# Kernel optimization log

Hardware: AMD Instinct MI355X
Metric: run time of the kernel (lower is better)

## Reference

```python
import jax, jax.numpy as jnp
import numpy as np

H, D = 16, 64  # heads, head dim; E = H*D


def setup_inputs() -> dict:
    key = jax.random.key(0)
    ks = jax.random.split(key, 8)
    B, T, E = 4, 1024, 1024
    s = (2.0 / E) ** 0.5
    return {
        "x": jax.random.normal(ks[0], (B, T, E), jnp.float32),
        "wq": jax.random.normal(ks[1], (H * D, E), jnp.float32) * s,
        "wk": jax.random.normal(ks[2], (H * D, E), jnp.float32) * s,
        "wv": jax.random.normal(ks[3], (H * D, E), jnp.float32) * s,
        "wvr": jax.random.normal(ks[4], (H * D, E), jnp.float32) * s,
        "wr": jax.random.normal(ks[5], (H, E, T), jnp.float32) * s,
        "wj": jax.random.normal(ks[6], (E, E), jnp.float32) * s,
        "gate": jnp.zeros((H, 3), jnp.float32),
        "wo": jax.random.normal(ks[7], (E, H * D), jnp.float32) * s,
    }


def reference(x, wq, wk, wv, wvr, wr, wj, gate, wo):
    B, T, E = x.shape
    scale = 1.0 / D ** 0.5

    def proj(w):  # torch Linear: y = x @ w.T, then split heads -> (B,H,T,D)
        return jnp.einsum('bte,fe->btf', x, w).reshape(B, T, H, D).transpose(0, 2, 1, 3)

    mask = jnp.triu(jnp.ones((T, T), bool), 1)  # True above diagonal (masked)

    # --- branch 1: standard causal QKV attention ---
    q, k, v = proj(wq), proj(wk), proj(wv)
    s1 = jnp.einsum('bhid,bhjd->bhij', q, k) * scale
    a1 = jax.nn.softmax(jnp.where(mask, -jnp.inf, s1), axis=-1)
    out1 = jnp.einsum('bhij,bhjd->bhid', a1, v)

    # --- branch 2: RRPRAM (parameter-based per-key scores, broadcast over queries) ---
    rv = proj(wvr)
    s2 = jnp.einsum('bte,het->bht', x, wr[:, :, :T]) * scale  # score per key position
    s2 = jnp.broadcast_to(s2[:, :, None, :], (B, H, T, T))
    a2 = jax.nn.softmax(jnp.where(mask, -jnp.inf, s2), axis=-1)
    out2 = jnp.einsum('bhij,bhjd->bhid', a2, rv)

    # --- branch 3: Janus self-echo (rank-1 outer-product scores) ---
    echo = jnp.einsum('bte,fe->btf', x, wj)            # x @ wj.T
    echo_back = jnp.einsum('btf,fe->bte', echo, wj)    # echo @ wj
    sc = jnp.sum(x * echo_back, axis=-1) / (E ** 0.5)  # (B,T)
    s3 = sc[:, :, None] * sc[:, None, :]               # (B,T,T)
    a3 = jax.nn.softmax(jnp.where(mask, -jnp.inf, s3), axis=-1)
    jv = echo.reshape(B, T, H, D).transpose(0, 2, 1, 3)
    out3 = jnp.einsum('bij,bhjd->bhid', a3, jv)

    # --- gated combine (softmax over the 3 branches per head) ---
    g = jax.nn.softmax(gate, axis=-1)  # (H,3)
    out = (g[:, 0][None, :, None, None] * out1
           + g[:, 1][None, :, None, None] * out2
           + g[:, 2][None, :, None, None] * out3)
    out = out.transpose(0, 2, 1, 3).reshape(B, T, H * D)
    return jnp.einsum('btf,ef->bte', out, wo)
```

## Files before the change

kernel.cpp:

```cpp
#include <hip/hip_runtime.h>
#include <cstdint>
#include <cstddef>

typedef unsigned short u16;
typedef short bf16x8 __attribute__((ext_vector_type(8)));
typedef short bf16x4 __attribute__((ext_vector_type(4)));
typedef float f32x4 __attribute__((ext_vector_type(4)));

constexpr int B_ = 4, T_ = 1024, E_ = 1024, H_ = 16, D_ = 64;

__device__ __forceinline__ float bf2f(u16 u) {
  union { unsigned u; float f; } v; v.u = ((unsigned)u) << 16; return v.f;
}
__device__ __forceinline__ u16 f2bf(float f) {
  union { float f; unsigned u; } v; v.f = f;
  return (u16)((v.u + 0x7fffu + ((v.u >> 16) & 1u)) >> 16);
}

#define GLD_LDS16(gp, lp)                                                      \
  __builtin_amdgcn_global_load_lds(                                            \
      (const __attribute__((address_space(1))) void*)(gp),                     \
      (__attribute__((address_space(3))) void*)(lp), 16, 0, 0)

#define SBAR()                                                                 \
  do {                                                                         \
    __builtin_amdgcn_sched_barrier(0);                                         \
    __builtin_amdgcn_s_barrier();                                              \
    __builtin_amdgcn_sched_barrier(0);                                         \
  } while (0)
#define WAIT_LGKM0()                                                           \
  do {                                                                         \
    asm volatile("s_waitcnt lgkmcnt(0)" ::: "memory");                         \
    __builtin_amdgcn_sched_barrier(0);                                         \
  } while (0)
#define WAIT_VM4()                                                             \
  do {                                                                         \
    asm volatile("s_waitcnt vmcnt(4)" ::: "memory");                           \
    __builtin_amdgcn_sched_barrier(0);                                         \
  } while (0)

__global__ __launch_bounds__(512, 2) void gemm_qkv8(
    const u16* __restrict__ A, const u16* __restrict__ Bm, u16* __restrict__ C)
{
  __shared__ u16 smem[65536];

  const int tid  = threadIdx.x;
  const int lane = tid & 63;
  const int wave = tid >> 6;
  const int wm = wave >> 2;
  const int wn = wave & 3;
  const int fr = lane & 15;
  const int fg = lane >> 4;
  const int fx = fr & 7;
  const int m0 = blockIdx.y * 256;
  const int n0 = blockIdx.x * 256;

  auto stage = [&](int ktl, int half) {
    const int buf = ktl & 1;
    int kt = (ktl > 15) ? 15 : ktl;
    const int k0 = kt << 6;
    const u16* src = (half < 2)
        ? (A  + (size_t)(m0 + (half & 1) * 128) * 1024)
        : (Bm + (size_t)(n0 + (half & 1) * 128) * 1024);
    u16* dst = smem + (buf << 15) + (half << 13);
    #pragma unroll
    for (int l = 0; l < 2; l++) {
      const int s = (l << 9) | tid;
      const int r = s >> 3, ch = s & 7;
      GLD_LDS16(src + (size_t)r * 1024 + k0 + ((ch ^ (r & 7)) << 3), dst + s * 8);
    }
  };

  f32x4 acc[8][4];
  #pragma unroll
  for (int i = 0; i < 8; i++)
    #pragma unroll
    for (int j = 0; j < 4; j++) acc[i][j] = f32x4{0.f, 0.f, 0.f, 0.f};

  stage(0, 0); stage(0, 1); stage(0, 2); stage(0, 3);
  stage(1, 2); stage(1, 0);
  WAIT_VM4();
  __builtin_amdgcn_s_barrier();
  __builtin_amdgcn_sched_barrier(0);

  const int ko0 = (fg ^ fx) << 3;
  const int ko1 = ((4 | fg) ^ fx) << 3;

  for (int t = 0; t < 16; t++) {
    const int buf = t & 1;
    const int ab = (buf << 15) + (wm << 13) + fr * 64;
    const int bb = (buf << 15) + 16384 + (wn << 12) + fr * 64;

    bf16x8 aF[4][2], bF[4][2];

    #pragma unroll
    for (int mt = 0; mt < 4; mt++) {
      aF[mt][0] = *(const bf16x8*)(smem + ab + mt * 1024 + ko0);
      aF[mt][1] = *(const bf16x8*)(smem + ab + mt * 1024 + ko1);
    }
    #pragma unroll
    for (int nt = 0; nt < 2; nt++) {
      bF[nt][0] = *(const bf16x8*)(smem + bb + nt * 1024 + ko0);
      bF[nt][1] = *(const bf16x8*)(smem + bb + nt * 1024 + ko1);
    }
    stage(t + 1, 1);
    SBAR();
    WAIT_LGKM0();
    __builtin_amdgcn_s_setprio(1);
    #pragma unroll
    for (int mt = 0; mt < 4; mt++)
      #pragma unroll
      for (int nt = 0; nt < 2; nt++) {
        acc[mt][nt] = __builtin_amdgcn_mfma_f32_16x16x32_bf16(aF[mt][0], bF[nt][0], acc[mt][nt], 0, 0, 0);
        acc[mt][nt] = __builtin_amdgcn_mfma_f32_16x16x32_bf16(aF[mt][1], bF[nt][1], acc[mt][nt], 0, 0, 0);
      }
    __builtin_amdgcn_s_setprio(0);
    SBAR();

    #pragma unroll
    for (int nt = 2; nt < 4; nt++) {
      bF[nt][0] = *(const bf16x8*)(smem + bb + nt * 1024 + ko0);
      bF[nt][1] = *(const bf16x8*)(smem + bb + nt * 1024 + ko1);
    }
    stage(t + 1, 3);
    SBAR();
    WAIT_LGKM0();
    __builtin_amdgcn_s_setprio(1);
    #pragma unroll
    for (int mt = 0; mt < 4; mt++)
      #pragma unroll
      for (int nt = 2; nt < 4; nt++) {
        acc[mt][nt] = __builtin_amdgcn_mfma_f32_16x16x32_bf16(aF[mt][0], bF[nt][0], acc[mt][nt], 0, 0, 0);
        acc[mt][nt] = __builtin_amdgcn_mfma_f32_16x16x32_bf16(aF[mt][1], bF[nt][1], acc[mt][nt], 0, 0, 0);
      }
    __builtin_amdgcn_s_setprio(0);
    SBAR();

    #pragma unroll
    for (int mt = 0; mt < 4; mt++) {
      aF[mt][0] = *(const bf16x8*)(smem + ab + (4 + mt) * 1024 + ko0);
      aF[mt][1] = *(const bf16x8*)(smem + ab + (4 + mt) * 1024 + ko1);
    }
    stage(t + 2, 2);
    SBAR();
    WAIT_LGKM0();
    __builtin_amdgcn_s_setprio(1);
    #pragma unroll
    for (int mt = 0; mt < 4; mt++)
      #pragma unroll
      for (int nt = 0; nt < 2; nt++) {
        acc[4 + mt][nt] = __builtin_amdgcn_mfma_f32_16x16x32_bf16(aF[mt][0], bF[nt][0], acc[4 + mt][nt], 0, 0, 0);
        acc[4 + mt][nt] = __builtin_amdgcn_mfma_f32_16x16x32_bf16(aF[mt][1], bF[nt][1], acc[4 + mt][nt], 0, 0, 0);
      }
    __builtin_amdgcn_s_setprio(0);
    SBAR();

    stage(t + 2, 0);
    SBAR();
    __builtin_amdgcn_s_setprio(1);
    #pragma unroll
    for (int mt = 0; mt < 4; mt++)
      #pragma unroll
      for (int nt = 2; nt < 4; nt++) {
        acc[4 + mt][nt] = __builtin_amdgcn_mfma_f32_16x16x32_bf16(aF[mt][0], bF[nt][0], acc[4 + mt][nt], 0, 0, 0);
        acc[4 + mt][nt] = __builtin_amdgcn_mfma_f32_16x16x32_bf16(aF[mt][1], bF[nt][1], acc[4 + mt][nt], 0, 0, 0);
      }
    __builtin_amdgcn_s_setprio(0);
    WAIT_VM4();
    __builtin_amdgcn_s_barrier();
    __builtin_amdgcn_sched_barrier(0);
  }

  u16* Cp = C + (size_t)(m0 + wm * 128) * 4096 + n0 + wn * 64;
  #pragma unroll
  for (int mt = 0; mt < 8; mt++)
    #pragma unroll
    for (int nt = 0; nt < 4; nt++)
      #pragma unroll
      for (int r2 = 0; r2 < 4; r2++)
        Cp[(size_t)(mt * 16 + fg * 4 + r2) * 4096 + nt * 16 + fr] = f2bf(acc[mt][nt][r2]);
}

template<int WM, int WN, int MT, int NT, bool CBF16>
__global__ __launch_bounds__(WM * WN * 64) void gemm_bt(
    const u16* __restrict__ A, const u16* __restrict__ Bm,
    void* __restrict__ Cv, int N, int K,
    int lda, int ldb, int ldc,
    long batchA, long batchB, long batchC, float alpha)
{
  constexpr int TM = WM * MT * 16;
  constexpr int TN = WN * NT * 16;
  constexpr int THREADS = WM * WN * 64;
  constexpr int ASZ = TM * 32, BSZ = TN * 32;

  __shared__ u16 smem[ASZ + BSZ];
  u16* sA = smem;
  u16* sB = smem + ASZ;

  const int z = blockIdx.z;
  const u16* Ab = A + (size_t)z * batchA;
  const u16* Bb = Bm + (size_t)z * batchB;
  const int m0 = blockIdx.y * TM;
  const int n0 = blockIdx.x * TN;
  const int tid = threadIdx.x;
  const int lane = tid & 63;
  const int wave = tid >> 6;
  const int wm = wave % WM;
  const int wn = wave / WM;
  const int fr = lane & 15;
  const int fg = lane >> 4;

  f32x4 acc[MT][NT];
  const f32x4 zero = {0.f, 0.f, 0.f, 0.f};
  #pragma unroll
  for (int i = 0; i < MT; i++)
    #pragma unroll
    for (int j = 0; j < NT; j++) acc[i][j] = zero;

  for (int k0 = 0; k0 < K; k0 += 32) {
    __syncthreads();
    for (int s = tid; s < TM * 4; s += THREADS) {
      const int row = s >> 2, ch = s & 3;
      GLD_LDS16(Ab + (size_t)(m0 + row) * lda + k0 + ch * 8, &sA[s * 8]);
    }
    for (int s = tid; s < TN * 4; s += THREADS) {
      const int row = s >> 2, ch = s & 3;
      int rr = n0 + row; if (rr > N - 1) rr = N - 1;
      GLD_LDS16(Bb + (size_t)rr * ldb + k0 + ch * 8, &sB[s * 8]);
    }
    __syncthreads();

    bf16x8 av[MT], bv[NT];
    #pragma unroll
    for (int mt = 0; mt < MT; mt++)
      av[mt] = *(const bf16x8*)&sA[((wm * MT + mt) * 16 + fr) * 32 + fg * 8];
    #pragma unroll
    for (int nt = 0; nt < NT; nt++)
      bv[nt] = *(const bf16x8*)&sB[((wn * NT + nt) * 16 + fr) * 32 + fg * 8];
    #pragma unroll
    for (int mt = 0; mt < MT; mt++)
      #pragma unroll
      for (int nt = 0; nt < NT; nt++)
        acc[mt][nt] = __builtin_amdgcn_mfma_f32_16x16x32_bf16(av[mt], bv[nt], acc[mt][nt], 0, 0, 0);
  }

  const int er = (lane >> 4) * 4;
  const int ec = lane & 15;
  #pragma unroll
  for (int mt = 0; mt < MT; mt++) {
    #pragma unroll
    for (int nt = 0; nt < NT; nt++) {
      const int row = m0 + (wm * MT + mt) * 16 + er;
      const int col = n0 + (wn * NT + nt) * 16 + ec;
      if (col < N) {
        #pragma unroll
        for (int r2 = 0; r2 < 4; r2++) {
          const float vv = acc[mt][nt][r2] * alpha;
          const size_t ci = (size_t)z * batchC + (size_t)(row + r2) * ldc + col;
          if constexpr (CBF16) ((u16*)Cv)[ci] = f2bf(vv);
          else                 ((float*)Cv)[ci] = vv;
        }
      }
    }
  }
}

__global__ __launch_bounds__(512, 2) void gemm_echo8(
    const u16* __restrict__ A, const u16* __restrict__ Alo,
    const u16* __restrict__ Bm, const u16* __restrict__ Blo,
    u16* __restrict__ echoT, float* __restrict__ sc)
{
  __shared__ u16 smem[65536];

  const int tid  = threadIdx.x;
  const int lane = tid & 63;
  const int wave = tid >> 6;
  const int wm = wave >> 2;
  const int wn = wave & 3;
  const int fr = lane & 15;
  const int fg = lane >> 4;
  const int fx = fr & 7;
  const int m0 = blockIdx.y * 128;
  const int n0 = blockIdx.x * 128;

  auto stage = [&](int ktl, int unit) {
    const int buf = ktl & 1;
    int kt = (ktl > 15) ? 15 : ktl;
    const int k0 = kt << 6;
    const u16* src = (unit == 0) ? A   + (size_t)m0 * 1024
                   : (unit == 1) ? Alo + (size_t)m0 * 1024
                   : (unit == 2) ? Bm  + (size_t)n0 * 1024
                   :               Blo + (size_t)n0 * 1024;
    u16* dst = smem + (buf << 15) + (unit << 13);
    #pragma unroll
    for (int l = 0; l < 2; l++) {
      const int s = (l << 9) | tid;
      const int r = s >> 3, ch = s & 7;
      GLD_LDS16(src + (size_t)r * 1024 + k0 + ((ch ^ (r & 7)) << 3), dst + s * 8);
    }
  };

  f32x4 acc[4][2];
  #pragma unroll
  for (int i = 0; i < 4; i++)
    #pragma unroll
    for (int j = 0; j < 2; j++) acc[i][j] = f32x4{0.f, 0.f, 0.f, 0.f};

  stage(0, 0); stage(0, 1); stage(0, 2); stage(0, 3);
  stage(1, 0); stage(1, 1);
  WAIT_VM4();
  __builtin_amdgcn_s_barrier();
  __builtin_amdgcn_sched_barrier(0);

  const int ko0 = (fg ^ fx) << 3;
  const int ko1 = ((4 | fg) ^ fx) << 3;

  for (int t = 0; t < 16; t++) {
    const int buf = t & 1;
    const int ab = (buf << 15) + (wm * 64 + fr) * 64;
    const int bb = (buf << 15) + 16384 + (wn * 32 + fr) * 64;

    bf16x8 aH[4][2], aL[4][2], bH, bL;

    #pragma unroll
    for (int mt = 0; mt < 4; mt++) {
      aH[mt][0] = *(const bf16x8*)(smem + ab + mt * 1024 + ko0);
      aH[mt][1] = *(const bf16x8*)(smem + ab + mt * 1024 + ko1);
      aL[mt][0] = *(const bf16x8*)(smem + ab + 8192 + mt * 1024 + ko0);
      aL[mt][1] = *(const bf16x8*)(smem + ab + 8192 + mt * 1024 + ko1);
    }
    bH = *(const bf16x8*)(smem + bb + ko0);
    bL = *(const bf16x8*)(smem + bb + 8192 + ko0);
    stage(t + 1, 2);
    SBAR();
    WAIT_LGKM0();
    __builtin_amdgcn_s_setprio(1);
    #pragma unroll
    for (int mt = 0; mt < 4; mt++) {
      acc[mt][0] = __builtin_amdgcn_mfma_f32_16x16x32_bf16(aH[mt][0], bH, acc[mt][0], 0, 0, 0);
      acc[mt][0] = __builtin_amdgcn_mfma_f32_16x16x32_bf16(aL[mt][0], bH, acc[mt][0], 0, 0, 0);
      acc[mt][0] = __builtin_amdgcn_mfma_f32_16x16x32_bf16(aH[mt][0], bL, acc[mt][0], 0, 0, 0);
    }
    __builtin_amdgcn_s_setprio(0);
    SBAR();

    bH = *(const bf16x8*)(smem + bb + ko1);
    bL = *(const bf16x8*)(smem + bb + 8192 + ko1);
    stage(t + 1, 3);
    SBAR();
    WAIT_LGKM0();
    __builtin_amdgcn_s_setprio(1);
    #pragma unroll
    for (int mt = 0; mt < 4; mt++) {
      acc[mt][0] = __builtin_amdgcn_mfma_f32_16x16x32_bf16(aH[mt][1], bH, acc[mt][0], 0, 0, 0);
      acc[mt][0] = __builtin_amdgcn_mfma_f32_16x16x32_bf16(aL[mt][1], bH, acc[mt][0], 0, 0, 0);
      acc[mt][0] = __builtin_amdgcn_mfma_f32_16x16x32_bf16(aH[mt][1], bL, acc[mt][0], 0, 0, 0);
    }
    __builtin_amdgcn_s_setprio(0);
    SBAR();

    bH = *(const bf16x8*)(smem + bb + 1024 + ko0);
    bL = *(const bf16x8*)(smem + bb + 8192 + 1024 + ko0);
    stage(t + 2, 0);
    SBAR();
    WAIT_LGKM0();
    __builtin_amdgcn_s_setprio(1);
    #pragma unroll
    for (int mt = 0; mt < 4; mt++) {
      acc[mt][1] = __builtin_amdgcn_mfma_f32_16x16x32_bf16(aH[mt][0], bH, acc[mt][1], 0, 0, 0);
      acc[mt][1] = __builtin_amdgcn_mfma_f32_16x16x32_bf16(aL[mt][0], bH, acc[mt][1], 0, 0, 0);
      acc[mt][1] = __builtin_amdgcn_mfma_f32_16x16x32_bf16(aH[mt][0], bL, acc[mt][1], 0, 0, 0);
    }
    __builtin_amdgcn_s_setprio(0);
    SBAR();

    bH = *(const bf16x8*)(smem + bb + 1024 + ko1);
    bL = *(const bf16x8*)(smem + bb + 8192 + 1024 + ko1);
    stage(t + 2, 1);
    SBAR();
    WAIT_LGKM0();
    __builtin_amdgcn_s_setprio(1);
    #pragma unroll
    for (int mt = 0; mt < 4; mt++) {
      acc[mt][1] = __builtin_amdgcn_mfma_f32_16x16x32_bf16(aH[mt][1], bH, acc[mt][1], 0, 0, 0);
      acc[mt][1] = __builtin_amdgcn_mfma_f32_16x16x32_bf16(aL[mt][1], bH, acc[mt][1], 0, 0, 0);
      acc[mt][1] = __builtin_amdgcn_mfma_f32_16x16x32_bf16(aH[mt][1], bL, acc[mt][1], 0, 0, 0);
    }
    __builtin_amdgcn_s_setprio(0);
    WAIT_VM4();
    __builtin_amdgcn_s_barrier();
    __builtin_amdgcn_sched_barrier(0);
  }

  asm volatile("s_waitcnt vmcnt(0) lgkmcnt(0)" ::: "memory");
  __builtin_amdgcn_sched_barrier(0);
  __builtin_amdgcn_s_barrier();
  __builtin_amdgcn_sched_barrier(0);

  const int b   = m0 >> 10;
  const int t0l = m0 & 1023;
  u16* lt = smem;

  #pragma unroll
  for (int mt = 0; mt < 4; mt++) {
    float sq[4] = {0.f, 0.f, 0.f, 0.f};
    #pragma unroll
    for (int nt = 0; nt < 2; nt++) {
      const int cl = wn * 32 + nt * 16 + fr;
      #pragma unroll
      for (int r2 = 0; r2 < 4; r2++) {
        const float vv = acc[mt][nt][r2];
        sq[r2] += vv * vv;
        lt[cl * 132 + wm * 64 + mt * 16 + fg * 4 + r2] = f2bf(vv);
      }
    }
    #pragma unroll
    for (int m2 = 1; m2 < 16; m2 <<= 1) {
      sq[0] += __shfl_xor(sq[0], m2, 64);
      sq[1] += __shfl_xor(sq[1], m2, 64);
      sq[2] += __shfl_xor(sq[2], m2, 64);
      sq[3] += __shfl_xor(sq[3], m2, 64);
    }
    if (fr == 0) {
      #pragma unroll
      for (int r2 = 0; r2 < 4; r2++)
        atomicAdd(&sc[(size_t)b * T_ + t0l + wm * 64 + mt * 16 + fg * 4 + r2], sq[r2]);
    }
  }
  __syncthreads();
  for (int s = tid; s < 128 * 128; s += 512) {
    const int f = s >> 7, tt = s & 127;
    echoT[((size_t)b * E_ + n0 + f) * T_ + t0l + tt] = lt[f * 132 + tt];
  }
}

__global__ __launch_bounds__(512, 2) void flash1p(
    const u16* __restrict__ qkvr, const u16* __restrict__ vTb, u16* __restrict__ out1) {
  const int x = blockIdx.x, h = blockIdx.y, b = blockIdx.z;
  const int tid = threadIdx.x, lane = tid & 63, w = tid >> 6;
  const int fr = lane & 15, fg = lane >> 4;
  const int itA = x, itB = 7 - x;

  __shared__ u16 sQ[8192];
  __shared__ u16 sK[2][8192];
  __shared__ u16 sV[2][8192];

  const u16* Kb = qkvr + (size_t)(b * T_) * 4096 + 1024 + h * 64;
  const u16* Vb = vTb + (size_t)(b * H_ + h) * (D_ * T_);

  auto stageQ = [&](int it) {
    const u16* Qb = qkvr + ((size_t)(b * T_) + it * 128) * 4096 + h * 64;
    #pragma unroll
    for (int s0 = 0; s0 < 1024; s0 += 512) {
      const int s = s0 + tid;
      const int l = s & 63, g = s >> 6;
      const int row = (g >> 1) * 16 + (l & 15);
      const int c8  = (g & 1) * 4 + (l >> 4);
      GLD_LDS16(Qb + (size_t)row * 4096 + c8 * 8, &sQ[s * 8]);
    }
  };
  auto stageKV = [&](int jt, int bi) {
    #pragma unroll
    for (int s0 = 0; s0 < 1024; s0 += 512) {
      const int s = s0 + tid;
      const int l = s & 63, g = s >> 6;
      const int row = (g >> 1) * 16 + (l & 15);
      const int c8  = (g & 1) * 4 + (l >> 4);
      GLD_LDS16(Kb + (size_t)(jt * 128 + row) * 4096 + c8 * 8, &sK[bi][s * 8]);
    }
    #pragma unroll
    for (int s0 = 0; s0 < 1024; s0 += 512) {
      const int s = s0 + tid;
      const int jc = s >> 6, d = s & 63;
      GLD_LDS16(Vb + ((size_t)(jt * 16 + jc)) * 512 + d * 8, &sV[bi][s * 8]);
    }
  };

  stageQ(itA);
  stageKV(0, 0);
  asm volatile("s_waitcnt vmcnt(0)" ::: "memory");
  __syncthreads();

  bf16x8 bQ[2];
  f32x4 accO[4];
  float mrow, lrow;

  #pragma unroll 1
  for (int ph = 0; ph < 2; ph++) {
    const int it    = ph ? itB : itA;
    const int sbase = ph ? (itA + 1) : 0;

    #pragma unroll
    for (int kk = 0; kk < 2; kk++)
      bQ[kk] = *(const bf16x8*)&sQ[((((w * 2) + kk) << 6) | lane) * 8];
    mrow = -3.0e38f; lrow = 0.f;
    #pragma unroll
    for (int nd = 0; nd < 4; nd++) accO[nd] = f32x4{0.f, 0.f, 0.f, 0.f};

    for (int jt = 0; jt <= it; jt++) {
      const int bi = (sbase + jt) & 1;

      if (jt < it) {
        stageKV(jt + 1, bi ^ 1);
      } else if (ph == 0) {
        stageQ(itB);
        stageKV(0, bi ^ 1);
      }

      f32x4 accST[8];
      #pragma unroll
      for (int nf = 0; nf < 8; nf++) accST[nf] = f32x4{0.f, 0.f, 0.f, 0.f};
      #pragma unroll
      for (int kk = 0; kk < 2; kk++) {
        #pragma unroll
        for (int nf = 0; nf < 8; nf++) {
          const bf16x8 aK = *(const bf16x8*)&sK[bi][((((nf << 1) | kk) << 6) | lane) * 8];
          accST[nf] = __builtin_amdgcn_mfma_f32_16x16x32_bf16(aK, bQ[kk], accST[nf], 0, 0, 0);
        }
      }

      const bool diag = (jt == it);
      const int iloc = w * 16 + fr;
      float sv[8][4];
      float rmax = -3.0e38f;
      #pragma unroll
      for (int nf = 0; nf < 8; nf++)
        #pragma unroll
        for (int r = 0; r < 4; r++) {
          float s = accST[nf][r] * 0.125f;
          if (diag && (nf * 16 + fg * 4 + r) > iloc) s = -3.0e38f;
          sv[nf][r] = s;
          rmax = fmaxf(rmax, s);
        }
      rmax = fmaxf(rmax, __shfl_xor(rmax, 16, 64));
      rmax = fmaxf(rmax, __shfl_xor(rmax, 32, 64));
      const float mn = fmaxf(mrow, rmax);
      const float al = __expf(mrow - mn);
      mrow = mn;
      float ps = 0.f;
      bf16x4 pf[8];
      #pragma unroll
      for (int nf = 0; nf < 8; nf++)
        #pragma unroll
        for (int r = 0; r < 4; r++) {
          const float pv = __expf(sv[nf][r] - mn);
          ps += pv;
          pf[nf][r] = (short)f2bf(pv);
        }
      ps += __shfl_xor(ps, 16, 64);
      ps += __shfl_xor(ps, 32, 64);
      lrow = lrow * al + ps;
      #pragma unroll
      for (int r = 0; r < 4; r++) {
        const float alr = __shfl(al, fg * 4 + r, 64);
        #pragma unroll
        for (int nd = 0; nd < 4; nd++) accO[nd][r] *= alr;
      }

      #pragma unroll
      for (int kc = 0; kc < 8; kc++) {
        bf16x8 bV[4];
        #pragma unroll
        for (int nd = 0; nd < 4; nd++) {
          const bf16x4 vv = *(const bf16x4*)&sV[bi][
              (((kc * 2 + (fg >> 1)) * 64 + nd * 16 + fr) * 8) + (fg & 1) * 4];
          bV[nd] = bf16x8{vv[0], vv[1], vv[2], vv[3], 0, 0, 0, 0};
        }
        const bf16x4 pp = pf[kc];
        const bf16x8 pA = bf16x8{pp[0], pp[1], pp[2], pp[3], 0, 0, 0, 0};
        #pragma unroll
        for (int nd = 0; nd < 4; nd++)
          accO[nd] = __builtin_amdgcn_mfma_f32_16x16x32_bf16(pA, bV[nd], accO[nd], 0, 0, 0);
      }

      asm volatile("s_waitcnt vmcnt(0)" ::: "memory");
      __syncthreads();
    }

    u16* op = out1 + ((size_t)(b * T_) + it * 128) * E_ + h * 64;
    const float li = 1.0f / lrow;
    #pragma unroll
    for (int r = 0; r < 4; r++) {
      const float linv = __shfl(li, fg * 4 + r, 64);
      const int row = w * 16 + fg * 4 + r;
      #pragma unroll
      for (int nd = 0; nd < 4; nd++)
        op[(size_t)row * E_ + nd * 16 + fr] = f2bf(accO[nd][r] * linv);
    }
  }
}

__device__ __forceinline__ float block_max256(float v, float* red) {
  #pragma unroll
  for (int m = 32; m > 0; m >>= 1) v = fmaxf(v, __shfl_xor(v, m, 64));
  if ((threadIdx.x & 63) == 0) red[threadIdx.x >> 6] = v;
  __syncthreads();
  const float r = fmaxf(fmaxf(red[0], red[1]), fmaxf(red[2], red[3]));
  __syncthreads();
  return r;
}
__device__ __forceinline__ float block_sum256(float v, float* red) {
  #pragma unroll
  for (int m = 32; m > 0; m >>= 1) v += __shfl_xor(v, m, 64);
  if ((threadIdx.x & 63) == 0) red[threadIdx.x >> 6] = v;
  __syncthreads();
  const float r = (red[0] + red[1]) + (red[2] + red[3]);
  __syncthreads();
  return r;
}

__global__ __launch_bounds__(256) void cast_all(
    const float* __restrict__ x, const float* __restrict__ wq,
    const float* __restrict__ wk, const float* __restrict__ wv,
    const float* __restrict__ wvr, const float* __restrict__ wo,
    const float* __restrict__ wj,
    u16* __restrict__ xb, u16* __restrict__ xlo, u16* __restrict__ wcat,
    u16* __restrict__ wob, u16* __restrict__ wjb, u16* __restrict__ wjlo) {
  const int bid = blockIdx.x;
  if (bid < 4096) {
    const size_t i = ((size_t)bid * 256 + threadIdx.x) * 4;
    const float4 v = *(const float4*)(x + i);
    ushort4 oh, ol;
    oh.x = f2bf(v.x); ol.x = f2bf(v.x - bf2f(oh.x));
    oh.y = f2bf(v.y); ol.y = f2bf(v.y - bf2f(oh.y));
    oh.z = f2bf(v.z); ol.z = f2bf(v.z - bf2f(oh.z));
    oh.w = f2bf(v.w); ol.w = f2bf(v.w - bf2f(oh.w));
    *(ushort4*)(xb + i) = oh;
    *(ushort4*)(xlo + i) = ol;
  } else if (bid < 8192) {
    const int r = (bid - 4096) >> 10;
    const float* src = (r == 0) ? wq : (r == 1) ? wk : (r == 2) ? wv : wvr;
    const size_t i = ((size_t)((bid - 4096) & 1023) * 256 + threadIdx.x) * 4;
    const float4 v = *(const float4*)(src + i);
    ushort4 o;
    o.x = f2bf(v.x); o.y = f2bf(v.y); o.z = f2bf(v.z); o.w = f2bf(v.w);
    *(ushort4*)(wcat + (size_t)r * (1 << 20) + i) = o;
  } else if (bid < 9216) {
    const size_t i = ((size_t)(bid - 8192) * 256 + threadIdx.x) * 4;
    const float4 v = *(const float4*)(wo + i);
    ushort4 o;
    o.x = f2bf(v.x); o.y = f2bf(v.y); o.z = f2bf(v.z); o.w = f2bf(v.w);
    *(ushort4*)(wob + i) = o;
  } else {
    const size_t i = ((size_t)(bid - 9216) * 256 + threadIdx.x) * 4;
    const float4 v = *(const float4*)(wj + i);
    ushort4 oh, ol;
    oh.x = f2bf(v.x); ol.x = f2bf(v.x - bf2f(oh.x));
    oh.y = f2bf(v.y); ol.y = f2bf(v.y - bf2f(oh.y));
    oh.z = f2bf(v.z); ol.z = f2bf(v.z - bf2f(oh.z));
    oh.w = f2bf(v.w); ol.w = f2bf(v.w - bf2f(oh.w));
    *(ushort4*)(wjb + i) = oh;
    *(ushort4*)(wjlo + i) = ol;
  }
}

__global__ __launch_bounds__(256) void s2_direct(
    const u16* __restrict__ xb, const float* __restrict__ wr, float* __restrict__ s2) {
  const int t0 = blockIdx.x * 32, h = blockIdx.y;
  const int tt = threadIdx.x & 31, eg = threadIdx.x >> 5;
  float acc[4] = {0.f, 0.f, 0.f, 0.f};
  const float* wp = wr + (size_t)h * E_ * T_ + t0 + tt;
  for (int ec = 0; ec < 8; ec++) {
    const int e0 = ec * 128 + eg * 16;
    bf16x8 xv[4][2];
    #pragma unroll
    for (int b = 0; b < 4; b++) {
      const u16* xp = xb + ((size_t)(b * T_) + t0 + tt) * E_ + e0;
      xv[b][0] = *(const bf16x8*)xp;
      xv[b][1] = *(const bf16x8*)(xp + 8);
    }
    #pragma unroll
    for (int e2 = 0; e2 < 16; e2++) {
      const float w = wp[(size_t)(e0 + e2) * T_];
      #pragma unroll
      for (int b = 0; b < 4; b++)
        acc[b] += bf2f((u16)xv[b][e2 >> 3][e2 & 7]) * w;
    }
  }
  __shared__ float red[8][4][33];
  #pragma unroll
  for (int b = 0; b < 4; b++) red[eg][b][tt] = acc[b];
  __syncthreads();
  if (threadIdx.x < 128) {
    const int b = threadIdx.x >> 5, t = threadIdx.x & 31;
    float s = 0.f;
    #pragma unroll
    for (int g = 0; g < 8; g++) s += red[g][b][t];
    s2[((size_t)b * H_ + h) * T_ + t0 + t] = s * 0.125f;
  }
}

__global__ __launch_bounds__(256) void a3_softmax(const float* __restrict__ sc, u16* __restrict__ a3) {
  const int i = blockIdx.x;
  const int b = blockIdx.y;
  const float* sr = sc + (size_t)b * T_;
  const float sci = sr[i] * 0.03125f;
  u16* row = a3 + ((size_t)b * T_ + i) * T_;
  __shared__ float red[4];
  float v[4];
  float m = -3.0e38f;
  #pragma unroll
  for (int k = 0; k < 4; k++) {
    const int j = threadIdx.x + k * 256;
    const float xv = (j <= i) ? sci * (sr[j] * 0.03125f) : -3.0e38f;
    v[k] = xv;
    m = fmaxf(m, xv);
  }
  m = block_max256(m, red);
  float s = 0.f;
  #pragma unroll
  for (int k = 0; k < 4; k++) {
    const int j = threadIdx.x + k * 256;
    const float p = (j <= i) ? __expf(v[k] - m) : 0.f;
    v[k] = p;
    s += p;
  }
  s = block_sum256(s, red);
  const float inv = 1.0f / s;
  #pragma unroll
  for (int k = 0; k < 4; k++) {
    const int j = threadIdx.x + k * 256;
    row[j] = f2bf(v[k] * inv);
  }
}

__global__ __launch_bounds__(1024) void branch2_scan(
    const float* __restrict__ s2, const u16* __restrict__ rv, int ldrv,
    u16* __restrict__ out2) {
  const int h = blockIdx.x, b = blockIdx.y;
  const int tid = threadIdx.x;
  const int lane = tid & 63;
  const int wv = tid >> 6;

  const float* srow = s2 + ((size_t)b * H_ + h) * T_;

  __shared__ float wbuf[T_];
  __shared__ float numtot[16][64];
  __shared__ float dentot[16];
  __shared__ float redm[16];

  float m = srow[tid];
  #pragma unroll
  for (int mk = 32; mk > 0; mk >>= 1) m = fmaxf(m, __shfl_xor(m, mk, 64));
  if (lane == 0) redm[wv] = m;
  __syncthreads();
  m = redm[0];
  #pragma unroll
  for (int i2 = 1; i2 < 16; i2++) m = fmaxf(m, redm[i2]);

  wbuf[tid] = __expf(srow[tid] - m);
  __syncthreads();

  const u16* rvp = rv + (size_t)(b * T_) * ldrv + h * D_ + lane;
  const int j0 = wv * 64;
  float num = 0.f, den = 0.f;
  #pragma unroll 8
  for (int j2 = 0; j2 < 64; j2++) {
    const float w = wbuf[j0 + j2];
    den += w;
    num += w * bf2f(rvp[(size_t)(j0 + j2) * ldrv]);
  }
  numtot[wv][lane] = num;
  if (lane == 0) dentot[wv] = den;
  __syncthreads();

  float num_off = 0.f, den_off = 0.f;
  for (int w2 = 0; w2 < wv; w2++) {
    num_off += numtot[w2][lane];
    den_off += dentot[w2];
  }

  u16* op = out2 + (size_t)b * T_ * E_ + h * D_ + lane;
  num = num_off; den = den_off;
  #pragma unroll 8
  for (int j2 = 0; j2 < 64; j2++) {
    const float w = wbuf[j0 + j2];
    num += w * bf2f(rvp[(size_t)(j0 + j2) * ldrv]);
    den += w;
    op[(size_t)(j0 + j2) * E_] = f2bf(num / den);
  }
}

__global__ __launch_bounds__(256) void transpose_v(const u16* __restrict__ v, u16* __restrict__ vTb,
                                                   int ldv) {
  const int bh = blockIdx.x;
  const int b = bh >> 4, h = bh & 15;
  const int d0 = blockIdx.y * 32, t0 = blockIdx.z * 32;
  __shared__ u16 tile[32][33];
  const int c = threadIdx.x & 31, r0 = threadIdx.x >> 5;
  #pragma unroll
  for (int rr = 0; rr < 32; rr += 8) {
    const int t = t0 + rr + r0;
    tile[rr + r0][c] = v[((size_t)b * T_ + t) * ldv + h * 64 + d0 + c];
  }
  __syncthreads();
  #pragma unroll
  for (int rr = 0; rr < 32; rr += 8) {
    const int d = d0 + rr + r0;
    const int t = t0 + c;
    vTb[((size_t)(bh * 128 + (t >> 3)) * 64 + d) * 8 + (t & 7)] = tile[c][rr + r0];
  }
}

__global__ __launch_bounds__(256) void combine_gate(
    const u16* __restrict__ o1, const u16* __restrict__ o2, const u16* __restrict__ o3,
    const float* __restrict__ gate, u16* __restrict__ comb) {
  const size_t idx = (size_t)blockIdx.x * 256 + threadIdx.x;
  const int f = (int)(idx & (E_ - 1));
  const int h = f >> 6;
  const float g0 = gate[h * 3 + 0], g1 = gate[h * 3 + 1], g2 = gate[h * 3 + 2];
  const float mx = fmaxf(g0, fmaxf(g1, g2));
  const float e0 = __expf(g0 - mx), e1 = __expf(g1 - mx), e2 = __expf(g2 - mx);
  const float inv = 1.0f / (e0 + e1 + e2);
  const float o = (e0 * bf2f(o1[idx]) + e1 * bf2f(o2[idx]) + e2 * bf2f(o3[idx])) * inv;
  comb[idx] = f2bf(o);
}

extern "C" void kernel_launch(void* const* d_in, const int* in_sizes, int n_in,
                              void* d_out, int out_size, void* d_ws, size_t ws_size,
                              hipStream_t stream) {
  (void)in_sizes; (void)n_in; (void)out_size; (void)ws_size;
  const float* x    = (const float*)d_in[0];
  const float* wq   = (const float*)d_in[1];
  const float* wk   = (const float*)d_in[2];
  const float* wv   = (const float*)d_in[3];
  const float* wvr  = (const float*)d_in[4];
  const float* wr   = (const float*)d_in[5];
  const float* wj   = (const float*)d_in[6];
  const float* gate = (const float*)d_in[7];
  const float* wo   = (const float*)d_in[8];
  float* out = (float*)d_out;

  char* p = (char*)d_ws;
  auto alloc = [&](size_t bytes) -> char* {
    char* r = p; p += (bytes + 255) & ~(size_t)255; return r;
  };
  const size_t NTE = (size_t)B_ * T_ * E_;
  const size_t NW  = (size_t)E_ * E_;

  u16* xb    = (u16*)alloc(NTE * 2);
  u16* xlo   = (u16*)alloc(NTE * 2);
  u16* wcat  = (u16*)alloc(4 * NW * 2);
  u16* wjb   = (u16*)alloc(NW * 2);
  u16* wjlo  = (u16*)alloc(NW * 2);
  u16* wob   = (u16*)alloc(NW * 2);
  u16* qkvr  = (u16*)alloc(NTE * 4 * 2);
  u16* vT    = (u16*)alloc(NTE * 2);
  u16* echoT = (u16*)alloc(NTE * 2);
  u16* a3p   = (u16*)alloc(NTE * 2);
  float* sc  = (float*)alloc((size_t)B_ * T_ * 4);
  float* s2  = (float*)alloc((size_t)B_ * H_ * T_ * 4);
  u16* out1b = (u16*)alloc(NTE * 2);
  u16* out2b = (u16*)alloc(NTE * 2);
  u16* out3b = (u16*)alloc(NTE * 2);
  u16* comb  = (u16*)alloc(NTE * 2);

  cast_all<<<dim3(10240), 256, 0, stream>>>(x, wq, wk, wv, wvr, wo, wj,
                                            xb, xlo, wcat, wob, wjb, wjlo);
  hipMemsetAsync(sc, 0, (size_t)B_ * T_ * 4, stream);

  gemm_qkv8<<<dim3(16, 16), 512, 0, stream>>>(xb, wcat, qkvr);

  gemm_echo8<<<dim3(8, 32), 512, 0, stream>>>(xb, xlo, wjb, wjlo, echoT, sc);

  transpose_v<<<dim3(B_ * H_, D_ / 32, T_ / 32), 256, 0, stream>>>(qkvr + 2048, vT, 4096);
  s2_direct<<<dim3(T_ / 32, H_), 256, 0, stream>>>(xb, wr, s2);

  branch2_scan<<<dim3(H_, B_), 1024, 0, stream>>>(s2, qkvr + 3072, 4096, out2b);

  a3_softmax<<<dim3(T_, B_), 256, 0, stream>>>(sc, a3p);
  gemm_bt<2,2,4,2,true><<<dim3(E_ / 64, T_ / 128, B_), 256, 0, stream>>>(
      a3p, echoT, out3b, E_, T_, T_, T_, E_,
      (long)T_ * T_, (long)E_ * T_, (long)T_ * E_, 1.f);

  flash1p<<<dim3(4, H_, B_), 512, 0, stream>>>(qkvr, vT, out1b);

  combine_gate<<<dim3((unsigned)(NTE / 256)), 256, 0, stream>>>(out1b, out2b, out3b, gate, comb);
  gemm_bt<2,2,4,2,false><<<dim3(E_ / 64, (B_ * T_) / 128, 1), 256, 0, stream>>>(
      comb, wob, out, E_, E_, E_, E_, E_, 0L, 0L, 0L, 1.f);
}
```

Measured before the change: 352.9 us.

## Fuse V transpose into QKV GEMM epilogue and halve flash query tile

The QKV GEMM epilogue now also writes the V block directly in the packed transposed layout that the attention kernel consumes, so the separate transpose_v launch and its extra pass over V are removed. The causal flash attention kernel moves from 128-row query tiles with 512 threads to 64-row tiles with 256 threads. It launches twice as many blocks, still pairs a short and a long tile per block for load balance, and allows higher occupancy per CU. The trade-offs are extra scattered stores in the GEMM epilogue and reloading each K/V tile for more query blocks.

Measured after the change: 353.6 us. Within noise of the previous version (+0.2%).

```diff
diff --git a/kernel.cpp b/kernel.cpp
--- a/kernel.cpp
+++ b/kernel.cpp
@@ -40,7 +40,8 @@
   } while (0)
 
 __global__ __launch_bounds__(512, 2) void gemm_qkv8(
-    const u16* __restrict__ A, const u16* __restrict__ Bm, u16* __restrict__ C)
+    const u16* __restrict__ A, const u16* __restrict__ Bm, u16* __restrict__ C,
+    u16* __restrict__ vT)
 {
   __shared__ u16 smem[65536];
 
@@ -179,6 +180,24 @@
       #pragma unroll
       for (int r2 = 0; r2 < 4; r2++)
         Cp[(size_t)(mt * 16 + fg * 4 + r2) * 4096 + nt * 16 + fr] = f2bf(acc[mt][nt][r2]);
+
+  if ((unsigned)(n0 - 2048) < 1024u) {
+    const int b  = m0 >> 10;
+    const int t0 = (m0 & 1023) + wm * 128;
+    #pragma unroll
+    for (int mt = 0; mt < 8; mt++) {
+      const int tb3 = ((t0 + mt * 16) >> 3) + (fg >> 1);
+      #pragma unroll
+      for (int nt = 0; nt < 4; nt++) {
+        const int dcol = (n0 - 2048) + wn * 64 + nt * 16 + fr;
+        const int h = dcol >> 6, d = dcol & 63;
+        ushort4 pk;
+        pk.x = f2bf(acc[mt][nt][0]); pk.y = f2bf(acc[mt][nt][1]);
+        pk.z = f2bf(acc[mt][nt][2]); pk.w = f2bf(acc[mt][nt][3]);
+        *(ushort4*)&vT[(((size_t)(b * 16 + h) * 128 + tb3) * 64 + d) * 8 + (fg & 1) * 4] = pk;
+      }
+    }
+  }
 }
 
 template<int WM, int WN, int MT, int NT, bool CBF16>
@@ -434,14 +453,14 @@
   }
 }
 
-__global__ __launch_bounds__(512, 2) void flash1p(
+__global__ __launch_bounds__(256, 4) void flash1p2(
     const u16* __restrict__ qkvr, const u16* __restrict__ vTb, u16* __restrict__ out1) {
   const int x = blockIdx.x, h = blockIdx.y, b = blockIdx.z;
   const int tid = threadIdx.x, lane = tid & 63, w = tid >> 6;
   const int fr = lane & 15, fg = lane >> 4;
-  const int itA = x, itB = 7 - x;
-
-  __shared__ u16 sQ[8192];
+  const int itA = x, itB = 15 - x;
+
+  __shared__ u16 sQ[4096];
   __shared__ u16 sK[2][8192];
   __shared__ u16 sV[2][8192];
 
@@ -449,9 +468,9 @@
   const u16* Vb = vTb + (size_t)(b * H_ + h) * (D_ * T_);
 
   auto stageQ = [&](int it) {
-    const u16* Qb = qkvr + ((size_t)(b * T_) + it * 128) * 4096 + h * 64;
-    #pragma unroll
-    for (int s0 = 0; s0 < 1024; s0 += 512) {
+    const u16* Qb = qkvr + ((size_t)(b * T_) + it * 64) * 4096 + h * 64;
+    #pragma unroll
+    for (int s0 = 0; s0 < 512; s0 += 256) {
       const int s = s0 + tid;
       const int l = s & 63, g = s >> 6;
       const int row = (g >> 1) * 16 + (l & 15);
@@ -461,7 +480,7 @@
   };
   auto stageKV = [&](int jt, int bi) {
     #pragma unroll
-    for (int s0 = 0; s0 < 1024; s0 += 512) {
+    for (int s0 = 0; s0 < 1024; s0 += 256) {
       const int s = s0 + tid;
       const int l = s & 63, g = s >> 6;
       const int row = (g >> 1) * 16 + (l & 15);
@@ -469,7 +488,7 @@
       GLD_LDS16(Kb + (size_t)(jt * 128 + row) * 4096 + c8 * 8, &sK[bi][s * 8]);
     }
     #pragma unroll
-    for (int s0 = 0; s0 < 1024; s0 += 512) {
+    for (int s0 = 0; s0 < 1024; s0 += 256) {
       const int s = s0 + tid;
       const int jc = s >> 6, d = s & 63;
       GLD_LDS16(Vb + ((size_t)(jt * 16 + jc)) * 512 + d * 8, &sV[bi][s * 8]);
@@ -484,23 +503,24 @@
   bf16x8 bQ[2];
   f32x4 accO[4];
   float mrow, lrow;
+  int cnt = 0;
 
   #pragma unroll 1
   for (int ph = 0; ph < 2; ph++) {
-    const int it    = ph ? itB : itA;
-    const int sbase = ph ? (itA + 1) : 0;
+    const int it = ph ? itB : itA;
+    const int nsteps = (it >> 1) + 1;
 
     #pragma unroll
     for (int kk = 0; kk < 2; kk++)
-      bQ[kk] = *(const bf16x8*)&sQ[((((w * 2) + kk) << 6) | lane) * 8];
+      bQ[kk] = *(const bf16x8*)&sQ[(((w * 2 + kk) << 6) | lane) * 8];
     mrow = -3.0e38f; lrow = 0.f;
     #pragma unroll
     for (int nd = 0; nd < 4; nd++) accO[nd] = f32x4{0.f, 0.f, 0.f, 0.f};
 
-    for (int jt = 0; jt <= it; jt++) {
-      const int bi = (sbase + jt) & 1;
-
-      if (jt < it) {
+    for (int jt = 0; jt < nsteps; jt++, cnt++) {
+      const int bi = cnt & 1;
+
+      if (jt < nsteps - 1) {
         stageKV(jt + 1, bi ^ 1);
       } else if (ph == 0) {
         stageQ(itB);
@@ -519,8 +539,8 @@
         }
       }
 
-      const bool diag = (jt == it);
-      const int iloc = w * 16 + fr;
+      const bool diag = (jt == nsteps - 1);
+      const int iloc = it * 64 + w * 16 + fr;
       float sv[8][4];
       float rmax = -3.0e38f;
       #pragma unroll
@@ -528,7 +548,7 @@
         #pragma unroll
         for (int r = 0; r < 4; r++) {
           float s = accST[nf][r] * 0.125f;
-          if (diag && (nf * 16 + fg * 4 + r) > iloc) s = -3.0e38f;
+          if (diag && (jt * 128 + nf * 16 + fg * 4 + r) > iloc) s = -3.0e38f;
           sv[nf][r] = s;
           rmax = fmaxf(rmax, s);
         }
@@ -577,7 +597,7 @@
       __syncthreads();
     }
 
-    u16* op = out1 + ((size_t)(b * T_) + it * 128) * E_ + h * 64;
+    u16* op = out1 + ((size_t)(b * T_) + it * 64) * E_ + h * 64;
     const float li = 1.0f / lrow;
     #pragma unroll
     for (int r = 0; r < 4; r++) {
@@ -781,27 +801,6 @@
   }
 }
 
-__global__ __launch_bounds__(256) void transpose_v(const u16* __restrict__ v, u16* __restrict__ vTb,
-                                                   int ldv) {
-  const int bh = blockIdx.x;
-  const int b = bh >> 4, h = bh & 15;
-  const int d0 = blockIdx.y * 32, t0 = blockIdx.z * 32;
-  __shared__ u16 tile[32][33];
-  const int c = threadIdx.x & 31, r0 = threadIdx.x >> 5;
-  #pragma unroll
-  for (int rr = 0; rr < 32; rr += 8) {
-    const int t = t0 + rr + r0;
-    tile[rr + r0][c] = v[((size_t)b * T_ + t) * ldv + h * 64 + d0 + c];
-  }
-  __syncthreads();
-  #pragma unroll
-  for (int rr = 0; rr < 32; rr += 8) {
-    const int d = d0 + rr + r0;
-    const int t = t0 + c;
-    vTb[((size_t)(bh * 128 + (t >> 3)) * 64 + d) * 8 + (t & 7)] = tile[c][rr + r0];
-  }
-}
-
 __global__ __launch_bounds__(256) void combine_gate(
     const u16* __restrict__ o1, const u16* __restrict__ o2, const u16* __restrict__ o3,
     const float* __restrict__ gate, u16* __restrict__ comb) {
@@ -859,11 +858,10 @@
                                             xb, xlo, wcat, wob, wjb, wjlo);
   hipMemsetAsync(sc, 0, (size_t)B_ * T_ * 4, stream);
 
-  gemm_qkv8<<<dim3(16, 16), 512, 0, stream>>>(xb, wcat, qkvr);
+  gemm_qkv8<<<dim3(16, 16), 512, 0, stream>>>(xb, wcat, qkvr, vT);
 
   gemm_echo8<<<dim3(8, 32), 512, 0, stream>>>(xb, xlo, wjb, wjlo, echoT, sc);
 
-  transpose_v<<<dim3(B_ * H_, D_ / 32, T_ / 32), 256, 0, stream>>>(qkvr + 2048, vT, 4096);
   s2_direct<<<dim3(T_ / 32, H_), 256, 0, stream>>>(xb, wr, s2);
 
   branch2_scan<<<dim3(H_, B_), 1024, 0, stream>>>(s2, qkvr + 3072, 4096, out2b);
@@ -873,7 +871,7 @@
       a3p, echoT, out3b, E_, T_, T_, T_, E_,
       (long)T_ * T_, (long)E_ * T_, (long)T_ * E_, 1.f);
 
-  flash1p<<<dim3(4, H_, B_), 512, 0, stream>>>(qkvr, vT, out1b);
+  flash1p2<<<dim3(8, H_, B_), 256, 0, stream>>>(qkvr, vT, out1b);
 
   combine_gate<<<dim3((unsigned)(NTE / 256)), 256, 0, stream>>>(out1b, out2b, out3b, gate, comb);
   gemm_bt<2,2,4,2,false><<<dim3(E_ / 64, (B_ * T_) / 128, 1), 256, 0, stream>>>(
```
